# Performance work log

Hardware: AMD Instinct MI355X
Metric: run time of the kernel (lower is better)

The kernel has to match this reference:

```python
import jax, jax.numpy as jnp
import numpy as np

H = 16
D_MODEL = 1024
D_K = D_MODEL // H


def setup_inputs() -> dict:
    key = jax.random.key(0)
    ks = jax.random.split(key, 12)
    B, S = 2, 2048
    scale = 1.0 / np.sqrt(D_MODEL)
    inp = {
        "query": jax.random.normal(ks[0], (B, S, D_MODEL), jnp.float32),
        "key": jax.random.normal(ks[1], (B, S, D_MODEL), jnp.float32),
        "value": jax.random.normal(ks[2], (B, S, D_MODEL), jnp.float32),
        "mask": jax.random.randint(ks[3], (B, S, S), 0, 2, jnp.int32),
        "w_q": jax.random.normal(ks[4], (D_MODEL, D_MODEL), jnp.float32) * scale,
        "b_q": jnp.zeros((D_MODEL,), jnp.float32),
        "w_k": jax.random.normal(ks[5], (D_MODEL, D_MODEL), jnp.float32) * scale,
        "b_k": jnp.zeros((D_MODEL,), jnp.float32),
        "w_v": jax.random.normal(ks[6], (D_MODEL, D_MODEL), jnp.float32) * scale,
        "b_v": jnp.zeros((D_MODEL,), jnp.float32),
        "w_o": jax.random.normal(ks[7], (D_MODEL, D_MODEL), jnp.float32) * scale,
        "b_o": jnp.zeros((D_MODEL,), jnp.float32),
    }
    return inp


def reference(query, key, value, mask, w_q, b_q, w_k, b_k, w_v, b_v, w_o, b_o):
    B, S, _ = query.shape
    # linear projections (torch nn.Linear: x @ W^T + b)
    q = query @ w_q.T + b_q
    k = key @ w_k.T + b_k
    v = value @ w_v.T + b_v
    # split heads -> [B, H, S, D_K]
    q = q.reshape(B, S, H, D_K).transpose(0, 2, 1, 3)
    k = k.reshape(B, S, H, D_K).transpose(0, 2, 1, 3)
    v = v.reshape(B, S, H, D_K).transpose(0, 2, 1, 3)
    # scores [B, H, S, S]; original masks BEFORE dividing by sqrt(d_k)
    scores = jnp.einsum("bhqd,bhkd->bhqk", q, k)
    m = mask[:, None, :, :]  # broadcast over heads (mask.unsqueeze(1))
    scores = jnp.where(m == 0, jnp.float32(-1e9), scores)
    scores = scores / jnp.sqrt(jnp.float32(D_K))
    attn = jax.nn.softmax(scores, axis=-1)
    # dropout is identity in eval mode
    ctx = jnp.einsum("bhqk,bhkd->bhqd", attn, v)
    ctx = ctx.transpose(0, 2, 1, 3).reshape(B, S, H * D_K)
    return ctx @ w_o.T + b_o
```

## Files before the change

### kernel.cpp

```cpp
#include <hip/hip_runtime.h>
#include <hip/hip_bf16.h>
#include <stdint.h>

typedef __attribute__((ext_vector_type(8))) short short8;
typedef __attribute__((ext_vector_type(4))) short short4v;
typedef __attribute__((ext_vector_type(4))) float f32x4;
typedef __attribute__((ext_vector_type(4))) unsigned short us4;
typedef unsigned short ushort_t;

#define LDS_AS __attribute__((address_space(3)))
#define GLB_AS __attribute__((address_space(1)))

__device__ __forceinline__ void gload_lds16(const void* g, void* l) {
    __builtin_amdgcn_global_load_lds((const GLB_AS uint32_t*)g, (LDS_AS uint32_t*)l, 16, 0, 0);
}

__device__ __forceinline__ unsigned short f2bf(float f) {
    union { float f; uint32_t u; } v; v.f = f;
    uint32_t r = v.u + 0x7FFFu + ((v.u >> 16) & 1u);
    return (unsigned short)(r >> 16);
}

__device__ __forceinline__ float fexp2(float x) {
#if __has_builtin(__builtin_amdgcn_exp2f)
    return __builtin_amdgcn_exp2f(x);
#else
    return exp2f(x);
#endif
}

__device__ __forceinline__ uint32_t fbits(float f) {
    union { float f; uint32_t u; } v; v.f = f; return v.u;
}

__device__ __forceinline__ f32x4 mfma32(short8 a, short8 b, f32x4 c) {
    return __builtin_amdgcn_mfma_f32_16x16x32_bf16(a, b, c, 0, 0, 0);
}
__device__ __forceinline__ f32x4 mfma16(short4v a, short4v b, f32x4 c) {
    return __builtin_amdgcn_mfma_f32_16x16x16bf16_1k(a, b, c, 0, 0, 0);
}

__device__ __forceinline__ short8 lds_frag(const char* base, int row, int kc) {
    int byte = row * 128 + ((kc ^ (row & 7)) << 4);
    return *(const short8*)(base + byte);
}

__global__ __launch_bounds__(256) void cvt_all(
    const float* p0, const float* p1, const float* p2, const float* p3,
    const float* p4, const float* p5, const float* p6,
    ushort_t* o0, ushort_t* o1, ushort_t* o2, ushort_t* o3,
    ushort_t* o4, ushort_t* o5, ushort_t* o6) {
    int z = blockIdx.y;
    const float* in = z == 0 ? p0 : z == 1 ? p1 : z == 2 ? p2 : z == 3 ? p3 : z == 4 ? p4 : z == 5 ? p5 : p6;
    ushort_t* out = z == 0 ? o0 : z == 1 ? o1 : z == 2 ? o2 : z == 3 ? o3 : z == 4 ? o4 : z == 5 ? o5 : o6;
    int n4 = z < 3 ? 1048576 : 262144;
    int i = blockIdx.x * 256 + threadIdx.x;
    int stride = gridDim.x * 256;
    for (; i < n4; i += stride) {
        float4 f = ((const float4*)in)[i];
        us4 o;
        o[0] = f2bf(f.x); o[1] = f2bf(f.y); o[2] = f2bf(f.z); o[3] = f2bf(f.w);
        ((us4*)out)[i] = o;
    }
}

__global__ __launch_bounds__(256) void pack_mask(const int* __restrict__ mask,
                                                 unsigned long long* __restrict__ out) {
    int i = blockIdx.x * 256 + threadIdx.x;
    unsigned long long bits = __ballot(mask[i] != 0);
    if ((threadIdx.x & 63) == 0) {
        int k = i & 2047, q = (i >> 11) & 2047, b = i >> 22;
        out[((size_t)b * 32 + (k >> 6)) * 2048 + q] = bits;
    }
}

__device__ __forceinline__ void gemm_core(const ushort_t* Ab, const ushort_t* Wb,
                                          char* ldsA, char* ldsW, int tid, f32x4 acc[4][4]) {
    constexpr int K = 1024;
    int lane = tid & 63, wid = tid >> 6;
    int cl = lane & 15, gr = lane >> 4;
    int wm = (wid >> 1) * 64, wn = (wid & 1) * 64;
#pragma unroll
    for (int i = 0; i < 4; ++i)
#pragma unroll
        for (int j = 0; j < 4; ++j) acc[i][j] = (f32x4)0.0f;

    for (int kt = 0; kt < K / 64; ++kt) {
        int k0 = kt * 64;
#pragma unroll
        for (int iss = 0; iss < 4; ++iss) {
            int c = iss * 256 + tid;
            int r = c >> 3, kc = (c & 7) ^ (r & 7);
            gload_lds16(Ab + (size_t)r * K + k0 + kc * 8, ldsA + c * 16);
            gload_lds16(Wb + (size_t)r * K + k0 + kc * 8, ldsW + c * 16);
        }
        __syncthreads();
#pragma unroll
        for (int ks = 0; ks < 2; ++ks) {
            short8 af[4], wf[4];
#pragma unroll
            for (int t = 0; t < 4; ++t) {
                af[t] = lds_frag(ldsA, wm + t * 16 + cl, ks * 4 + gr);
                wf[t] = lds_frag(ldsW, wn + t * 16 + cl, ks * 4 + gr);
            }
#pragma unroll
            for (int i = 0; i < 4; ++i)
#pragma unroll
                for (int j = 0; j < 4; ++j)
                    acc[i][j] = mfma32(af[i], wf[j], acc[i][j]);
        }
        __syncthreads();
    }
}

__global__ __launch_bounds__(256)
void gemm3(const ushort_t* A0, const ushort_t* A1, const ushort_t* A2,
           const ushort_t* W0, const ushort_t* W1, const ushort_t* W2,
           const float* B0, const float* B1, const float* B2,
           void* O0, void* O1, void* O2, int mode_ovr, float scl0) {
    __shared__ char lds[32768];
    char* ldsA = lds;
    char* ldsW = lds + 16384;
    int z = blockIdx.z;
    const ushort_t* A = z == 0 ? A0 : z == 1 ? A1 : A2;
    const ushort_t* W = z == 0 ? W0 : z == 1 ? W1 : W2;
    const float* bias = z == 0 ? B0 : z == 1 ? B1 : B2;
    void* out = z == 0 ? O0 : z == 1 ? O1 : O2;
    int mode = mode_ovr >= 0 ? mode_ovr : (z == 2 ? 1 : 0);
    float scl = z == 0 ? scl0 : 1.0f;

    int tid = threadIdx.x, lane = tid & 63, wid = tid >> 6;
    int cl = lane & 15, gr = lane >> 4;
    int wm = (wid >> 1) * 64, wn = (wid & 1) * 64;
    int bm = blockIdx.y * 128, bn = blockIdx.x * 128;

    f32x4 acc[4][4];
    gemm_core(A + (size_t)bm * 1024, W + (size_t)bn * 1024, ldsA, ldsW, tid, acc);

#pragma unroll
    for (int j = 0; j < 4; ++j) {
        int n = bn + wn + j * 16 + cl;
        float bv = bias[n];
#pragma unroll
        for (int i = 0; i < 4; ++i) {
            int mbase = bm + wm + i * 16 + gr * 4;
            if (mode == 0) {
#pragma unroll
                for (int r = 0; r < 4; ++r) {
                    int m = mbase + r;
                    float v = (acc[i][j][r] + bv) * scl;
                    size_t idx = (((size_t)((m >> 11) * 16 + (n >> 6))) * 2048 + (m & 2047)) * 64 + (n & 63);
                    ((ushort_t*)out)[idx] = f2bf(v);
                }
            } else if (mode == 1) {
                us4 pk;
#pragma unroll
                for (int r = 0; r < 4; ++r) pk[r] = f2bf(acc[i][j][r] + bv);
                size_t idx = (((size_t)((mbase >> 11) * 16 + (n >> 6))) * 64 + (n & 63)) * 2048 + (mbase & 2047);
                *(us4*)((ushort_t*)out + idx) = pk;
            } else {
#pragma unroll
                for (int r = 0; r < 4; ++r)
                    ((float*)out)[(size_t)(mbase + r) * 1024 + n] = acc[i][j][r] + bv;
            }
        }
    }
}

__global__ __launch_bounds__(256, 4)
void attn(const ushort_t* __restrict__ Q, const ushort_t* __restrict__ Kh,
          const ushort_t* __restrict__ Vt, const unsigned long long* __restrict__ PM,
          ushort_t* __restrict__ ctx) {
    constexpr int S = 2048;
    __shared__ char lds[32768];
    int tid = threadIdx.x, lane = tid & 63, wid = tid >> 6;
    int cl = lane & 15, gr = lane >> 4, c7 = cl & 7;

    int blk = (blockIdx.x & 7) * 64 + (blockIdx.x >> 3);
    int bh = blk >> 4, qt = blk & 15;
    int b = bh >> 4, h = bh & 15;
    const ushort_t* Qb = Q + (size_t)bh * S * 64;
    const ushort_t* Kb = Kh + (size_t)bh * S * 64;
    const ushort_t* Vb = Vt + (size_t)bh * 64 * S;
    int q0w = qt * 128 + wid * 32;

    short8 qreg[2][2];
#pragma unroll
    for (int qf = 0; qf < 2; ++qf)
#pragma unroll
        for (int ks = 0; ks < 2; ++ks)
            qreg[qf][ks] = *(const short8*)(Qb + (size_t)(q0w + qf * 16 + cl) * 64 + ks * 32 + gr * 8);

    f32x4 acc[2][4];
    f32x4 accl[2];
#pragma unroll
    for (int qf = 0; qf < 2; ++qf) {
        accl[qf] = (f32x4)0.0f;
#pragma unroll
        for (int df = 0; df < 4; ++df) acc[qf][df] = (f32x4)0.0f;
    }

    int kOff[2], vOff[2], dstL[2];
#pragma unroll
    for (int iss = 0; iss < 2; ++iss) {
        int L = iss * 256 + tid;
        int r = L >> 3, c = (L & 7) ^ (r & 7);
        kOff[iss] = r * 64 + c * 8;
        vOff[iss] = r * S + c * 8;
        dstL[iss] = L * 16;
    }
    int aK0 = cl * 128 + ((0 * 4 + gr) ^ c7) * 16;
    int aK1 = cl * 128 + ((1 * 4 + gr) ^ c7) * 16;
    int aV[4];
#pragma unroll
    for (int nf = 0; nf < 4; ++nf)
        aV[nf] = cl * 128 + (((2 * nf) + (gr >> 1)) ^ c7) * 16 + (gr & 1) * 8;

    const unsigned long long* pmq = PM + (size_t)b * 32 * 2048 + q0w + cl;

    short4v ones;
#pragma unroll
    for (int r = 0; r < 4; ++r) ones[r] = (short)0x3F80;

    auto stage = [&](int kv2, char* dst) {
        const ushort_t* Ks = Kb + (size_t)kv2 * 4096;
        const ushort_t* Vs = Vb + (size_t)kv2 * 64;
#pragma unroll
        for (int iss = 0; iss < 2; ++iss) {
            gload_lds16(Ks + kOff[iss], dst + dstL[iss]);
            gload_lds16(Vs + vOff[iss], dst + 8192 + dstL[iss]);
        }
    };

    stage(0, lds);
    __syncthreads();

    for (int kv = 0; kv < 32; ++kv) {
        char* cb = lds + (kv & 1) * 16384;
        if (kv < 31) stage(kv + 1, lds + ((kv + 1) & 1) * 16384);

        unsigned long long w0 = pmq[(size_t)kv * 2048];
        unsigned long long w1 = pmq[(size_t)kv * 2048 + 16];

        f32x4 sc[2][4];
#pragma unroll
        for (int nf = 0; nf < 4; ++nf) {
            short8 k0 = *(const short8*)(cb + aK0 + nf * 2048);
            short8 k1 = *(const short8*)(cb + aK1 + nf * 2048);
#pragma unroll
            for (int qf = 0; qf < 2; ++qf) {
                f32x4 s = mfma32(k0, qreg[qf][0], (f32x4)0.0f);
                sc[qf][nf] = mfma32(k1, qreg[qf][1], s);
            }
        }

        short4v pk[2][4];
#pragma unroll
        for (int qf = 0; qf < 2; ++qf) {
            unsigned long long ws = (qf == 0 ? w0 : w1) >> (gr * 4);
            uint32_t lo = (uint32_t)ws, hi = (uint32_t)(ws >> 32);
#pragma unroll
            for (int nf = 0; nf < 4; ++nf) {
                uint32_t wb = nf < 2 ? lo : hi;
                uint32_t u[4];
#pragma unroll
                for (int r = 0; r < 4; ++r) {
                    uint32_t bit = wb & (1u << ((nf & 1) * 16 + r));
                    float sel = bit ? sc[qf][nf][r] : -1.0e9f;
                    u[r] = fbits(fexp2(sel)) + 0x8000u;
                }
                union { uint32_t d[2]; short4v v; } pp;
                pp.d[0] = __builtin_amdgcn_perm(u[1], u[0], 0x07060302u);
                pp.d[1] = __builtin_amdgcn_perm(u[3], u[2], 0x07060302u);
                pk[qf][nf] = pp.v;
            }
        }

#pragma unroll
        for (int nf = 0; nf < 4; ++nf) {
#pragma unroll
            for (int df = 0; df < 4; ++df) {
                short4v vf = *(const short4v*)(cb + 8192 + aV[nf] + df * 2048);
                acc[0][df] = mfma16(pk[0][nf], vf, acc[0][df]);
                acc[1][df] = mfma16(pk[1][nf], vf, acc[1][df]);
            }
            accl[0] = mfma16(pk[0][nf], ones, accl[0]);
            accl[1] = mfma16(pk[1][nf], ones, accl[1]);
        }
        __syncthreads();
    }

#pragma unroll
    for (int qf = 0; qf < 2; ++qf) {
        float inv[4];
#pragma unroll
        for (int r = 0; r < 4; ++r) inv[r] = 1.0f / accl[qf][r];
#pragma unroll
        for (int df = 0; df < 4; ++df)
#pragma unroll
            for (int r = 0; r < 4; ++r) {
                int q = q0w + qf * 16 + gr * 4 + r;
                int d = df * 16 + cl;
                ctx[((size_t)b * S + q) * 1024 + h * 64 + d] = f2bf(acc[qf][df][r] * inv[r]);
            }
    }
}

extern "C" void kernel_launch(void* const* d_in, const int* in_sizes, int n_in,
                              void* d_out, int out_size, void* d_ws, size_t ws_size,
                              hipStream_t stream) {
    const float* query = (const float*)d_in[0];
    const float* key   = (const float*)d_in[1];
    const float* value = (const float*)d_in[2];
    const int*   mask  = (const int*)d_in[3];
    const float* w_q = (const float*)d_in[4];
    const float* b_q = (const float*)d_in[5];
    const float* w_k = (const float*)d_in[6];
    const float* b_k = (const float*)d_in[7];
    const float* w_v = (const float*)d_in[8];
    const float* b_v = (const float*)d_in[9];
    const float* w_o = (const float*)d_in[10];
    const float* b_o = (const float*)d_in[11];

    char* ws = (char*)d_ws;
    const size_t MB = 1 << 20;
    ushort_t* xq  = (ushort_t*)(ws + 0 * MB);
    ushort_t* xk  = (ushort_t*)(ws + 8 * MB);
    ushort_t* xv  = (ushort_t*)(ws + 16 * MB);
    ushort_t* wq  = (ushort_t*)(ws + 24 * MB);
    ushort_t* wk  = (ushort_t*)(ws + 26 * MB);
    ushort_t* wv  = (ushort_t*)(ws + 28 * MB);
    ushort_t* wo  = (ushort_t*)(ws + 30 * MB);
    ushort_t* qhm = (ushort_t*)(ws + 32 * MB);
    ushort_t* khm = (ushort_t*)(ws + 40 * MB);
    ushort_t* vt  = (ushort_t*)(ws + 48 * MB);
    unsigned long long* pm = (unsigned long long*)(ws + 56 * MB);
    ushort_t* ctx = (ushort_t*)(ws + 0 * MB);

    const float QSCALE = 0.125f * 1.44269504088896f;

    cvt_all<<<dim3(1024, 7), 256, 0, stream>>>(query, key, value, w_q, w_k, w_v, w_o,
                                               xq, xk, xv, wq, wk, wv, wo);
    pack_mask<<<32768, 256, 0, stream>>>(mask, pm);

    gemm3<<<dim3(8, 32, 3), 256, 0, stream>>>(xq, xk, xv, wq, wk, wv, b_q, b_k, b_v,
                                              qhm, khm, vt, -1, QSCALE);

    attn<<<512, 256, 0, stream>>>(qhm, khm, vt, pm, ctx);

    gemm3<<<dim3(8, 32, 1), 256, 0, stream>>>(ctx, ctx, ctx, wo, wo, wo, b_o, b_o, b_o,
                                              d_out, d_out, d_out, 2, 1.0f);
}
```

Measured before the change: 163.5 us.

## Split attention KV range across two wave halves and reduce through LDS

The attention kernel now launches 512 threads per block. Two groups of four waves each process half of the 32 KV tiles with their own double-buffered LDS region, then combine partial accumulators and row sums through shared memory before normalizing. This doubles the waves per query tile to improve latency hiding and shortens the serial KV loop. The cost is 64KB of LDS per block, which limits occupancy, plus an extra reduction step. The softmax stays unnormalized without a max subtraction, so summing the two halves is exact.

```diff
diff --git a/kernel.cpp b/kernel.cpp
--- a/kernel.cpp
+++ b/kernel.cpp
@@ -167,14 +167,16 @@
     }
 }
 
-__global__ __launch_bounds__(256, 4)
+__global__ __launch_bounds__(512, 4)
 void attn(const ushort_t* __restrict__ Q, const ushort_t* __restrict__ Kh,
           const ushort_t* __restrict__ Vt, const unsigned long long* __restrict__ PM,
           ushort_t* __restrict__ ctx) {
     constexpr int S = 2048;
-    __shared__ char lds[32768];
+    __shared__ char lds[65536];
     int tid = threadIdx.x, lane = tid & 63, wid = tid >> 6;
     int cl = lane & 15, gr = lane >> 4, c7 = cl & 7;
+    int h2 = wid & 1;
+    int qg = wid >> 1;
 
     int blk = (blockIdx.x & 7) * 64 + (blockIdx.x >> 3);
     int bh = blk >> 4, qt = blk & 15;
@@ -182,7 +184,7 @@
     const ushort_t* Qb = Q + (size_t)bh * S * 64;
     const ushort_t* Kb = Kh + (size_t)bh * S * 64;
     const ushort_t* Vb = Vt + (size_t)bh * 64 * S;
-    int q0w = qt * 128 + wid * 32;
+    int q0w = qt * 128 + qg * 32;
 
     short8 qreg[2][2];
 #pragma unroll
@@ -200,15 +202,18 @@
         for (int df = 0; df < 4; ++df) acc[qf][df] = (f32x4)0.0f;
     }
 
+    int hs = tid >> 8, stid = tid & 255;
     int kOff[2], vOff[2], dstL[2];
 #pragma unroll
     for (int iss = 0; iss < 2; ++iss) {
-        int L = iss * 256 + tid;
+        int L = iss * 256 + stid;
         int r = L >> 3, c = (L & 7) ^ (r & 7);
         kOff[iss] = r * 64 + c * 8;
         vOff[iss] = r * S + c * 8;
         dstL[iss] = L * 16;
     }
+    char* sbase = lds + hs * 32768;
+
     int aK0 = cl * 128 + ((0 * 4 + gr) ^ c7) * 16;
     int aK1 = cl * 128 + ((1 * 4 + gr) ^ c7) * 16;
     int aV[4];
@@ -222,9 +227,10 @@
 #pragma unroll
     for (int r = 0; r < 4; ++r) ones[r] = (short)0x3F80;
 
-    auto stage = [&](int kv2, char* dst) {
-        const ushort_t* Ks = Kb + (size_t)kv2 * 4096;
-        const ushort_t* Vs = Vb + (size_t)kv2 * 64;
+    auto stage = [&](int T, int parity) {
+        const ushort_t* Ks = Kb + (size_t)T * 4096;
+        const ushort_t* Vs = Vb + (size_t)T * 64;
+        char* dst = sbase + parity * 16384;
 #pragma unroll
         for (int iss = 0; iss < 2; ++iss) {
             gload_lds16(Ks + kOff[iss], dst + dstL[iss]);
@@ -232,15 +238,17 @@
         }
     };
 
-    stage(0, lds);
+    stage(hs * 16, 0);
     __syncthreads();
 
-    for (int kv = 0; kv < 32; ++kv) {
-        char* cb = lds + (kv & 1) * 16384;
-        if (kv < 31) stage(kv + 1, lds + ((kv + 1) & 1) * 16384);
-
-        unsigned long long w0 = pmq[(size_t)kv * 2048];
-        unsigned long long w1 = pmq[(size_t)kv * 2048 + 16];
+    char* mybase = lds + h2 * 32768;
+    for (int t = 0; t < 16; ++t) {
+        char* cb = mybase + (t & 1) * 16384;
+        if (t < 15) stage(hs * 16 + t + 1, (t + 1) & 1);
+
+        int kvi = h2 * 16 + t;
+        unsigned long long w0 = pmq[(size_t)kvi * 2048];
+        unsigned long long w1 = pmq[(size_t)kvi * 2048 + 16];
 
         f32x4 sc[2][4];
 #pragma unroll
@@ -290,19 +298,40 @@
         __syncthreads();
     }
 
-#pragma unroll
-    for (int qf = 0; qf < 2; ++qf) {
-        float inv[4];
-#pragma unroll
-        for (int r = 0; r < 4; ++r) inv[r] = 1.0f / accl[qf][r];
-#pragma unroll
-        for (int df = 0; df < 4; ++df)
-#pragma unroll
-            for (int r = 0; r < 4; ++r) {
-                int q = q0w + qf * 16 + gr * 4 + r;
-                int d = df * 16 + cl;
-                ctx[((size_t)b * S + q) * 1024 + h * 64 + d] = f2bf(acc[qf][df][r] * inv[r]);
-            }
+    if (h2) {
+        float* dst = (float*)(lds + qg * 10240 + lane * 160);
+#pragma unroll
+        for (int qf = 0; qf < 2; ++qf) {
+#pragma unroll
+            for (int df = 0; df < 4; ++df)
+                *(f32x4*)(dst + qf * 16 + df * 4) = acc[qf][df];
+            *(f32x4*)(dst + 32 + qf * 4) = accl[qf];
+        }
+    }
+    __syncthreads();
+    if (!h2) {
+        const float* src = (const float*)(lds + qg * 10240 + lane * 160);
+#pragma unroll
+        for (int qf = 0; qf < 2; ++qf) {
+#pragma unroll
+            for (int df = 0; df < 4; ++df)
+                acc[qf][df] += *(const f32x4*)(src + qf * 16 + df * 4);
+            accl[qf] += *(const f32x4*)(src + 32 + qf * 4);
+        }
+#pragma unroll
+        for (int qf = 0; qf < 2; ++qf) {
+            float inv[4];
+#pragma unroll
+            for (int r = 0; r < 4; ++r) inv[r] = 1.0f / accl[qf][r];
+#pragma unroll
+            for (int df = 0; df < 4; ++df)
+#pragma unroll
+                for (int r = 0; r < 4; ++r) {
+                    int q = q0w + qf * 16 + gr * 4 + r;
+                    int d = df * 16 + cl;
+                    ctx[((size_t)b * S + q) * 1024 + h * 64 + d] = f2bf(acc[qf][df][r] * inv[r]);
+                }
+        }
     }
 }
 
@@ -346,7 +375,7 @@
     gemm3<<<dim3(8, 32, 3), 256, 0, stream>>>(xq, xk, xv, wq, wk, wv, b_q, b_k, b_v,
                                               qhm, khm, vt, -1, QSCALE);
 
-    attn<<<512, 256, 0, stream>>>(qhm, khm, vt, pm, ctx);
+    attn<<<512, 512, 0, stream>>>(qhm, khm, vt, pm, ctx);
 
     gemm3<<<dim3(8, 32, 1), 256, 0, stream>>>(ctx, ctx, ctx, wo, wo, wo, b_o, b_o, b_o,
                                               d_out, d_out, d_out, 2, 1.0f);
```

Result: no change. 160.4 us (-1.9%).
